# Performance work log

Measured on AMD Instinct MI355X. Metric: run time of the kernel, lower is better.

The kernel has to match this reference:

```python
import jax, jax.numpy as jnp
import numpy as np

BETA = 0.25
GAMMA = 0.9
EPS = 1e-05
B, H, W, D, K = 64, 32, 32, 256, 1024


def setup_inputs() -> dict:
    key = jax.random.key(0)
    k1, k2 = jax.random.split(key)
    return {
        "inputs": jax.random.normal(k1, (B, H, W, D), dtype=jnp.float32),
        "codebook": jax.random.normal(k2, (D, K), dtype=jnp.float32),
        "ema_hidden_cluster": jnp.zeros((K,), dtype=jnp.float32),
        "ema_hidden_dw": jnp.zeros((D, K), dtype=jnp.float32),
        "counter": 1,  # counter after increment (fresh state: 0 + 1)
    }


def reference(inputs, codebook, ema_hidden_cluster, ema_hidden_dw, counter):
    d, k = codebook.shape
    flat = inputs.reshape(-1, d)  # [N, D]
    distances = (
        jnp.sum(jnp.square(flat), 1, keepdims=True)
        - 2.0 * jnp.matmul(flat, codebook)
        + jnp.sum(jnp.square(codebook), 0, keepdims=True)
    )
    encoding_indices = jnp.argmin(distances, axis=1)  # [N]
    encodings = jax.nn.one_hot(encoding_indices, k, dtype=distances.dtype)  # [N, K]
    flat_quantized = jnp.take(codebook, encoding_indices, axis=1).swapaxes(1, 0)  # [N, D]
    quantized = flat_quantized.reshape(inputs.shape)
    loss = BETA * jnp.mean(jnp.square(jax.lax.stop_gradient(quantized) - inputs))

    # --- EMA codebook update (training=True path) ---
    decay = jnp.float32(GAMMA)
    one = jnp.float32(1.0)
    bias = one - jnp.power(decay, counter)
    cluster_size = jnp.sum(encodings, axis=0)  # [K]
    hid_cs = ema_hidden_cluster * decay + cluster_size * (one - decay)
    avg_cs = hid_cs / bias
    dw = jnp.matmul(flat.T, encodings)  # [D, K]
    hid_dw = ema_hidden_dw * decay + dw * (one - decay)
    avg_dw = hid_dw / bias
    n = jnp.sum(avg_cs)
    smoothed_cs = (avg_cs + EPS) / (n + k * EPS) * n
    new_codebook = avg_dw / smoothed_cs[None, :]

    ste = inputs + jax.lax.stop_gradient(quantized - inputs)
    avg_probs = jnp.mean(encodings, 0)
    perplexity = jnp.exp(-jnp.sum(avg_probs * jnp.log(avg_probs + 1e-10)))
    return (ste, perplexity, loss, new_codebook)
```

## Files before the change

### kernel.cpp

```cpp
#include <hip/hip_runtime.h>

#define N 65536
#define D 256
#define K 1024
#define BETA 0.25f
#define GAMMA 0.9f
#define EPS 1e-5f

#define DWROWS 64

#define OFF_INDICES 0
#define OFF_PERM    262144
#define OFF_COUNTS  524288
#define OFF_CNORM   528384
#define OFF_OFFSETS 532480
#define OFF_CURSOR  536576
#define OFF_SMOOTH  540672
#define OFF_LOSSP   544768
#define OFF_CBT     546816
#define OFF_CBE     1595392

typedef __bf16 bf16x8 __attribute__((ext_vector_type(8)));
typedef short  s16x8  __attribute__((ext_vector_type(8)));
typedef float  f32x4  __attribute__((ext_vector_type(4)));

__device__ inline unsigned short f32_to_bf16_rn(float f) {
    unsigned int u = __float_as_uint(f);
    unsigned int r = u + 0x7fffu + ((u >> 16) & 1u);
    return (unsigned short)(r >> 16);
}

__device__ inline f32x4 mfma16(s16x8 a, s16x8 b, f32x4 c) {
    return __builtin_amdgcn_mfma_f32_16x16x32_bf16(
        __builtin_bit_cast(bf16x8, a), __builtin_bit_cast(bf16x8, b), c, 0, 0, 0);
}

__device__ __forceinline__ void stage16(const s16x8* __restrict__ g, s16x8* l) {
    __builtin_amdgcn_global_load_lds(
        (const __attribute__((address_space(1))) void*)g,
        (__attribute__((address_space(3))) void*)l, 16, 0, 0);
}

__global__ __launch_bounds__(256) void pack_cb(const float* __restrict__ cb,
                                               float* __restrict__ cbT,
                                               s16x8* __restrict__ cbEp,
                                               float* __restrict__ cnorm) {
    const int ct = blockIdx.x >> 2;
    const int c2 = blockIdx.x & 3;
#pragma unroll
    for (int it = 0; it < 2; ++it) {
        int u = it * 256 + threadIdx.x;
        int frgc = u >> 7;
        int ks = (u >> 6) & 1;
        int L = u & 63;
        int c = ct * 64 + frgc * 16 + (L & 15);
        int d0 = c2 * 64 + (ks * 4 + (L >> 4)) * 8;
        float v[8];
        s16x8 hv, lv;
        float ss = 0.f;
#pragma unroll
        for (int j = 0; j < 8; ++j) {
            float f = cb[(size_t)(d0 + j) * K + c];
            v[j] = f;
            unsigned short h = f32_to_bf16_rn(f);
            hv[j] = (short)h;
            lv[j] = (short)f32_to_bf16_rn(f - __uint_as_float((unsigned)h << 16));
            ss = fmaf(f, f, ss);
        }
        *(float4*)&cbT[(size_t)c * D + d0]     = make_float4(v[0], v[1], v[2], v[3]);
        *(float4*)&cbT[(size_t)c * D + d0 + 4] = make_float4(v[4], v[5], v[6], v[7]);
        cbEp[(size_t)(ct * 8 + c2) * 512 + u]     = hv;
        cbEp[(size_t)(ct * 8 + 4 + c2) * 512 + u] = lv;
        atomicAdd(&cnorm[c], ss);
    }
}

__global__ __launch_bounds__(256, 2) void argmin_mfma_kernel(
        const float* __restrict__ x,
        const s16x8* __restrict__ cbEp,
        const float* __restrict__ cnorm,
        int* __restrict__ indices,
        int* __restrict__ counts) {
    __shared__ s16x8 Bs[2][1024];

    const int tid = threadIdx.x;
    const int lane = tid & 63;
    const int w = tid >> 6;
    const int r0 = blockIdx.x * 128;
    const int row16 = lane & 15;
    const int quad = lane >> 4;

#pragma unroll
    for (int i = 0; i < 4; ++i)
        stage16(cbEp + i * 256 + tid, &Bs[0][i * 256 + w * 64]);

    s16x8 Ah[2][8], Al[2][8];
#pragma unroll
    for (int frg = 0; frg < 2; ++frg) {
#pragma unroll
        for (int kb8 = 0; kb8 < 8; ++kb8) {
            const float* src = &x[(size_t)(r0 + w * 32 + frg * 16 + row16) * D
                                  + kb8 * 32 + quad * 8];
            float4 v0 = *(const float4*)src;
            float4 v1 = *(const float4*)(src + 4);
            float f[8] = {v0.x, v0.y, v0.z, v0.w, v1.x, v1.y, v1.z, v1.w};
            s16x8 hv, lv;
#pragma unroll
            for (int j = 0; j < 8; ++j) {
                unsigned short h = f32_to_bf16_rn(f[j]);
                hv[j] = (short)h;
                lv[j] = (short)f32_to_bf16_rn(f[j] - __uint_as_float((unsigned)h << 16));
            }
            Ah[frg][kb8] = hv;
            Al[frg][kb8] = lv;
        }
    }

    float minv[2][4];
    int   mini[2][4];
#pragma unroll
    for (int frg = 0; frg < 2; ++frg)
#pragma unroll
        for (int reg = 0; reg < 4; ++reg) { minv[frg][reg] = 3.4e38f; mini[frg][reg] = 0; }

    for (int ct = 0; ct < 16; ++ct) {
        f32x4 acc[2][4];
#pragma unroll
        for (int frg = 0; frg < 2; ++frg)
#pragma unroll
            for (int fc = 0; fc < 4; ++fc) acc[frg][fc] = (f32x4){0.f, 0.f, 0.f, 0.f};

#pragma unroll
        for (int ph = 0; ph < 4; ++ph) {
            __syncthreads();
            const bool has_next = !(ct == 15 && ph == 3);
            if (has_next) {
                const int nct = (ph == 3) ? ct + 1 : ct;
                const int nph = (ph == 3) ? 0 : ph + 1;
                const size_t gb = (size_t)(nct * 8 + nph * 2) * 512;
#pragma unroll
                for (int i = 0; i < 4; ++i)
                    stage16(cbEp + gb + i * 256 + tid, &Bs[(ph + 1) & 1][i * 256 + w * 64]);
            }
#pragma unroll
            for (int half = 0; half < 2; ++half) {
                const int cchunk = ph * 2 + half;
                const int c2 = cchunk & 3;
#pragma unroll
                for (int ks = 0; ks < 2; ++ks) {
                    const int ksb = c2 * 2 + ks;
#pragma unroll
                    for (int fc = 0; fc < 4; ++fc) {
                        s16x8 b = Bs[ph & 1][half * 512 + (fc * 2 + ks) * 64 + lane];
#pragma unroll
                        for (int frg = 0; frg < 2; ++frg) {
                            acc[frg][fc] = mfma16(Ah[frg][ksb], b, acc[frg][fc]);
                            if (cchunk < 4)
                                acc[frg][fc] = mfma16(Al[frg][ksb], b, acc[frg][fc]);
                        }
                    }
                }
            }
        }
#pragma unroll
        for (int fc = 0; fc < 4; ++fc) {
            int col = ct * 64 + fc * 16 + row16;
            float cn = cnorm[col];
#pragma unroll
            for (int frg = 0; frg < 2; ++frg)
#pragma unroll
                for (int reg = 0; reg < 4; ++reg) {
                    float val = fmaf(-2.f, acc[frg][fc][reg], cn);
                    if (val < minv[frg][reg]) { minv[frg][reg] = val; mini[frg][reg] = col; }
                }
        }
    }

#pragma unroll
    for (int mask = 1; mask <= 8; mask <<= 1) {
#pragma unroll
        for (int frg = 0; frg < 2; ++frg)
#pragma unroll
            for (int reg = 0; reg < 4; ++reg) {
                float ov = __shfl_xor(minv[frg][reg], mask, 64);
                int   oi = __shfl_xor(mini[frg][reg], mask, 64);
                if (ov < minv[frg][reg] ||
                    (ov == minv[frg][reg] && oi < mini[frg][reg])) {
                    minv[frg][reg] = ov; mini[frg][reg] = oi;
                }
            }
    }
    if (row16 == 0) {
#pragma unroll
        for (int frg = 0; frg < 2; ++frg)
#pragma unroll
            for (int reg = 0; reg < 4; ++reg) {
                const int idx = mini[frg][reg];
                indices[r0 + w * 32 + frg * 16 + quad * 4 + reg] = idx;
                atomicAdd(&counts[idx], 1);
            }
    }
}

__global__ __launch_bounds__(1024) void finalize_kernel(const int* __restrict__ counts,
                                                        const float* __restrict__ ema_c,
                                                        const int* __restrict__ counter,
                                                        float* __restrict__ out_perp,
                                                        int* __restrict__ cursor,
                                                        float* __restrict__ smoothed) {
    const int k = threadIdx.x;
    __shared__ float fred[1024];
    __shared__ int scan[1024];
    __shared__ float nsum_s;

    const int c = counts[k];
    const float bias = 1.0f - powf(GAMMA, (float)counter[0]);
    const float hid = fmaf(ema_c[k], GAMMA, (float)c * (1.0f - GAMMA));
    const float avg = hid / bias;

    fred[k] = avg;
    __syncthreads();
    for (int s = 512; s >= 1; s >>= 1) {
        if (k < s) fred[k] += fred[k + s];
        __syncthreads();
    }
    if (k == 0) nsum_s = fred[0];
    __syncthreads();
    const float nsum = nsum_s;

    float p = (float)c * (1.0f / (float)N);
    fred[k] = p * logf(p + 1e-10f);
    __syncthreads();
    for (int s = 512; s >= 1; s >>= 1) {
        if (k < s) fred[k] += fred[k + s];
        __syncthreads();
    }
    if (k == 0) out_perp[0] = expf(-fred[0]);

    scan[k] = c;
    __syncthreads();
    for (int s = 1; s < 1024; s <<= 1) {
        int v = (k >= s) ? scan[k - s] : 0;
        __syncthreads();
        scan[k] += v;
        __syncthreads();
    }
    cursor[k] = scan[k] - c;

    smoothed[k] = (avg + EPS) / (nsum + (float)K * EPS) * nsum;
}

__global__ __launch_bounds__(256) void scatter_kernel(const int* __restrict__ indices,
                                                      int* __restrict__ cursor,
                                                      int* __restrict__ permk,
                                                      float* __restrict__ dwT) {
    const int n = blockIdx.x * 256 + threadIdx.x;
    *(float4*)&dwT[(size_t)n * 4] = make_float4(0.f, 0.f, 0.f, 0.f);
    const int k = indices[n];
    const int pos = atomicAdd(&cursor[k], 1);
    permk[pos] = n | (k << 16);
}

__global__ __launch_bounds__(256) void dw_fused_kernel(const float* __restrict__ x,
                                                       const float* __restrict__ cbT,
                                                       const int* __restrict__ permk,
                                                       float* __restrict__ ste,
                                                       float* __restrict__ dwT,
                                                       float* __restrict__ lossp) {
    __shared__ int s_rows[DWROWS];
    __shared__ int s_keys[DWROWS + 1];
    const int d = threadIdx.x;
    const int base = blockIdx.x * DWROWS;
    if (threadIdx.x < DWROWS) {
        const int pk = permk[base + threadIdx.x];
        s_rows[threadIdx.x] = pk & 0xffff;
        s_keys[threadIdx.x] = pk >> 16;
    }
    if (threadIdx.x == 0) s_keys[DWROWS] = -1;
    __syncthreads();
    float acc = 0.f;
    float ls = 0.f;
#pragma unroll 4
    for (int i = 0; i < DWROWS; ++i) {
        const int n = s_rows[i];
        const int k = s_keys[i];
        const float xv = x[(size_t)n * D + d];
        const float q  = cbT[(size_t)k * D + d];
        ste[(size_t)n * D + d] = q;
        acc += xv;
        const float df = q - xv;
        ls = fmaf(df, df, ls);
        if (s_keys[i + 1] != k) {
            atomicAdd(&dwT[(size_t)k * D + d], acc);
            acc = 0.f;
        }
    }
#pragma unroll
    for (int off = 32; off >= 1; off >>= 1) ls += __shfl_down(ls, off, 64);
    __shared__ float red[4];
    if ((d & 63) == 0) red[d >> 6] = ls;
    __syncthreads();
    if (d == 0) lossp[blockIdx.x] = red[0] + red[1] + red[2] + red[3];
}

__global__ __launch_bounds__(256) void codebook_final_kernel(const float* __restrict__ dwT,
                                                             const float* __restrict__ ema_dw,
                                                             const float* __restrict__ smoothed,
                                                             const int* __restrict__ counter,
                                                             const float* __restrict__ lossp,
                                                             float* __restrict__ out_cb,
                                                             float* __restrict__ out_loss) {
    __shared__ float tile[64][65];
    __shared__ float lred[4];
    const int tid = threadIdx.x;

    if (blockIdx.x == 0) {
        float s = lossp[tid] + lossp[tid + 256] + lossp[tid + 512] + lossp[tid + 768];
#pragma unroll
        for (int off = 32; off >= 1; off >>= 1) s += __shfl_down(s, off, 64);
        if ((tid & 63) == 0) lred[tid >> 6] = s;
        __syncthreads();
        if (tid == 0)
            out_loss[0] = BETA * (lred[0] + lred[1] + lred[2] + lred[3])
                          * (1.0f / ((float)N * (float)D));
        __syncthreads();
    }

    const int d0 = (blockIdx.x & 3) * 64;
    const int k0 = (blockIdx.x >> 2) * 64;
#pragma unroll
    for (int it = 0; it < 16; ++it) {
        int idx = it * 256 + tid;
        int kk = idx >> 6, dd = idx & 63;
        tile[kk][dd] = dwT[(size_t)(k0 + kk) * D + d0 + dd];
    }
    __syncthreads();
    const float bias = 1.0f - powf(GAMMA, (float)counter[0]);
#pragma unroll
    for (int it = 0; it < 16; ++it) {
        int idx = it * 256 + tid;
        int dd = idx >> 6, kk = idx & 63;
        float dwv = tile[kk][dd];
        float hid = fmaf(ema_dw[(size_t)(d0 + dd) * K + k0 + kk], GAMMA,
                         dwv * (1.0f - GAMMA));
        out_cb[(size_t)(d0 + dd) * K + k0 + kk] = (hid / bias) / smoothed[k0 + kk];
    }
}

extern "C" void kernel_launch(void* const* d_in, const int* in_sizes, int n_in,
                              void* d_out, int out_size, void* d_ws, size_t ws_size,
                              hipStream_t stream) {
    const float* x       = (const float*)d_in[0];
    const float* cb      = (const float*)d_in[1];
    const float* ema_c   = (const float*)d_in[2];
    const float* ema_dw  = (const float*)d_in[3];
    const int*   counter = (const int*)d_in[4];

    float* out = (float*)d_out;
    float* ste = out;
    float* out_perp = out + (size_t)N * D;
    float* out_loss = out_perp + 1;
    float* out_cb = out_perp + 2;

    char* ws = (char*)d_ws;
    int* indices  = (int*)(ws + OFF_INDICES);
    int* permk    = (int*)(ws + OFF_PERM);
    int* counts   = (int*)(ws + OFF_COUNTS);
    float* cnorm  = (float*)(ws + OFF_CNORM);
    int* cursor   = (int*)(ws + OFF_CURSOR);
    float* smooth = (float*)(ws + OFF_SMOOTH);
    float* cbT    = (float*)(ws + OFF_CBT);
    s16x8* cbEp   = (s16x8*)(ws + OFF_CBE);
    float* dwT    = (float*)(ws + OFF_CBE);
    float* lossp  = (float*)(ws + OFF_CNORM);

    hipMemsetAsync(counts, 0, 2 * K * sizeof(int), stream);

    pack_cb<<<64, 256, 0, stream>>>(cb, cbT, cbEp, cnorm);
    argmin_mfma_kernel<<<N / 128, 256, 0, stream>>>(x, cbEp, cnorm, indices, counts);
    finalize_kernel<<<1, 1024, 0, stream>>>(counts, ema_c, counter,
                                            out_perp, cursor, smooth);
    scatter_kernel<<<N / 256, 256, 0, stream>>>(indices, cursor, permk, dwT);
    dw_fused_kernel<<<N / DWROWS, 256, 0, stream>>>(x, cbT, permk, ste, dwT, lossp);
    codebook_final_kernel<<<64, 256, 0, stream>>>(dwT, ema_dw, smooth, counter,
                                                  lossp, out_cb, out_loss);
}
```

Before: 311.2 us.

## Replace sort-based dw accumulation with direct atomic scatter and fuse finalize

Removes the counting-sort pipeline (finalize scan, scatter, permuted dw kernel) and replaces it with one grid-stride kernel where each wavefront handles one row: it gathers the codeword into ste, atomically adds x into dwT per element, and counts cluster hits. The smoothing and perplexity reductions move into every codebook_final block, and the dwT zeroing becomes a memset. This cuts two kernel launches and the permutation traffic, but turns segment-reduced atomics into one float atomic per element (N*D atomics), which can contend heavily on popular codewords.

```diff
diff --git a/kernel.cpp b/kernel.cpp
--- a/kernel.cpp
+++ b/kernel.cpp
@@ -7,7 +7,7 @@
 #define GAMMA 0.9f
 #define EPS 1e-5f
 
-#define DWROWS 64
+#define TBLOCKS 512
 
 #define OFF_INDICES 0
 #define OFF_PERM    262144
@@ -79,8 +79,7 @@
         const float* __restrict__ x,
         const s16x8* __restrict__ cbEp,
         const float* __restrict__ cnorm,
-        int* __restrict__ indices,
-        int* __restrict__ counts) {
+        int* __restrict__ indices) {
     __shared__ s16x8 Bs[2][1024];
 
     const int tid = threadIdx.x;
@@ -194,136 +193,98 @@
 #pragma unroll
         for (int frg = 0; frg < 2; ++frg)
 #pragma unroll
-            for (int reg = 0; reg < 4; ++reg) {
-                const int idx = mini[frg][reg];
-                indices[r0 + w * 32 + frg * 16 + quad * 4 + reg] = idx;
-                atomicAdd(&counts[idx], 1);
-            }
-    }
-}
-
-__global__ __launch_bounds__(1024) void finalize_kernel(const int* __restrict__ counts,
-                                                        const float* __restrict__ ema_c,
-                                                        const int* __restrict__ counter,
-                                                        float* __restrict__ out_perp,
-                                                        int* __restrict__ cursor,
-                                                        float* __restrict__ smoothed) {
-    const int k = threadIdx.x;
-    __shared__ float fred[1024];
-    __shared__ int scan[1024];
-    __shared__ float nsum_s;
-
-    const int c = counts[k];
-    const float bias = 1.0f - powf(GAMMA, (float)counter[0]);
-    const float hid = fmaf(ema_c[k], GAMMA, (float)c * (1.0f - GAMMA));
-    const float avg = hid / bias;
-
-    fred[k] = avg;
-    __syncthreads();
-    for (int s = 512; s >= 1; s >>= 1) {
-        if (k < s) fred[k] += fred[k + s];
-        __syncthreads();
-    }
-    if (k == 0) nsum_s = fred[0];
-    __syncthreads();
-    const float nsum = nsum_s;
-
-    float p = (float)c * (1.0f / (float)N);
-    fred[k] = p * logf(p + 1e-10f);
-    __syncthreads();
-    for (int s = 512; s >= 1; s >>= 1) {
-        if (k < s) fred[k] += fred[k + s];
-        __syncthreads();
-    }
-    if (k == 0) out_perp[0] = expf(-fred[0]);
-
-    scan[k] = c;
-    __syncthreads();
-    for (int s = 1; s < 1024; s <<= 1) {
-        int v = (k >= s) ? scan[k - s] : 0;
-        __syncthreads();
-        scan[k] += v;
-        __syncthreads();
-    }
-    cursor[k] = scan[k] - c;
-
-    smoothed[k] = (avg + EPS) / (nsum + (float)K * EPS) * nsum;
-}
-
-__global__ __launch_bounds__(256) void scatter_kernel(const int* __restrict__ indices,
-                                                      int* __restrict__ cursor,
-                                                      int* __restrict__ permk,
-                                                      float* __restrict__ dwT) {
-    const int n = blockIdx.x * 256 + threadIdx.x;
-    *(float4*)&dwT[(size_t)n * 4] = make_float4(0.f, 0.f, 0.f, 0.f);
-    const int k = indices[n];
-    const int pos = atomicAdd(&cursor[k], 1);
-    permk[pos] = n | (k << 16);
-}
-
-__global__ __launch_bounds__(256) void dw_fused_kernel(const float* __restrict__ x,
-                                                       const float* __restrict__ cbT,
-                                                       const int* __restrict__ permk,
-                                                       float* __restrict__ ste,
-                                                       float* __restrict__ dwT,
-                                                       float* __restrict__ lossp) {
-    __shared__ int s_rows[DWROWS];
-    __shared__ int s_keys[DWROWS + 1];
-    const int d = threadIdx.x;
-    const int base = blockIdx.x * DWROWS;
-    if (threadIdx.x < DWROWS) {
-        const int pk = permk[base + threadIdx.x];
-        s_rows[threadIdx.x] = pk & 0xffff;
-        s_keys[threadIdx.x] = pk >> 16;
-    }
-    if (threadIdx.x == 0) s_keys[DWROWS] = -1;
-    __syncthreads();
-    float acc = 0.f;
+            for (int reg = 0; reg < 4; ++reg)
+                indices[r0 + w * 32 + frg * 16 + quad * 4 + reg] = mini[frg][reg];
+    }
+}
+
+__global__ __launch_bounds__(256) void tail_fused_kernel(const float* __restrict__ x,
+                                                         const float* __restrict__ cbT,
+                                                         const int* __restrict__ indices,
+                                                         float* __restrict__ ste,
+                                                         float* __restrict__ dwT,
+                                                         int* __restrict__ counts,
+                                                         float* __restrict__ lossp) {
+    const int lane = threadIdx.x & 63;
+    const int wid = (blockIdx.x * 256 + threadIdx.x) >> 6;
+    const int nwaves = TBLOCKS * 4;
+
     float ls = 0.f;
-#pragma unroll 4
-    for (int i = 0; i < DWROWS; ++i) {
-        const int n = s_rows[i];
-        const int k = s_keys[i];
-        const float xv = x[(size_t)n * D + d];
-        const float q  = cbT[(size_t)k * D + d];
-        ste[(size_t)n * D + d] = q;
-        acc += xv;
-        const float df = q - xv;
-        ls = fmaf(df, df, ls);
-        if (s_keys[i + 1] != k) {
-            atomicAdd(&dwT[(size_t)k * D + d], acc);
-            acc = 0.f;
-        }
+    for (int row = wid; row < N; row += nwaves) {
+        const int k = indices[row];
+        float4 q  = *(const float4*)&cbT[(size_t)k * D + lane * 4];
+        float4 xi = *(const float4*)&x[(size_t)row * D + lane * 4];
+        *(float4*)&ste[(size_t)row * D + lane * 4] = q;
+        float* dst = &dwT[(size_t)k * D + lane * 4];
+        atomicAdd(dst + 0, xi.x);
+        atomicAdd(dst + 1, xi.y);
+        atomicAdd(dst + 2, xi.z);
+        atomicAdd(dst + 3, xi.w);
+        float dx = q.x - xi.x, dy = q.y - xi.y, dz = q.z - xi.z, dw = q.w - xi.w;
+        ls = fmaf(dx, dx, ls); ls = fmaf(dy, dy, ls);
+        ls = fmaf(dz, dz, ls); ls = fmaf(dw, dw, ls);
+        if (lane == 0) atomicAdd(&counts[k], 1);
     }
 #pragma unroll
     for (int off = 32; off >= 1; off >>= 1) ls += __shfl_down(ls, off, 64);
     __shared__ float red[4];
-    if ((d & 63) == 0) red[d >> 6] = ls;
+    if ((threadIdx.x & 63) == 0) red[threadIdx.x >> 6] = ls;
     __syncthreads();
-    if (d == 0) lossp[blockIdx.x] = red[0] + red[1] + red[2] + red[3];
+    if (threadIdx.x == 0)
+        lossp[blockIdx.x] = red[0] + red[1] + red[2] + red[3];
 }
 
 __global__ __launch_bounds__(256) void codebook_final_kernel(const float* __restrict__ dwT,
                                                              const float* __restrict__ ema_dw,
-                                                             const float* __restrict__ smoothed,
+                                                             const int* __restrict__ counts,
+                                                             const float* __restrict__ ema_c,
                                                              const int* __restrict__ counter,
                                                              const float* __restrict__ lossp,
                                                              float* __restrict__ out_cb,
-                                                             float* __restrict__ out_loss) {
+                                                             float* __restrict__ out_loss,
+                                                             float* __restrict__ out_perp) {
     __shared__ float tile[64][65];
+    __shared__ float sm[1024];
+    __shared__ float wred[4][2];
     __shared__ float lred[4];
     const int tid = threadIdx.x;
+    const float bias = 1.0f - powf(GAMMA, (float)counter[0]);
+
+    float avg4[4];
+    float a = 0.f, e = 0.f;
+#pragma unroll
+    for (int i = 0; i < 4; ++i) {
+        const int k = i * 256 + tid;
+        const int c = counts[k];
+        const float avg = fmaf(ema_c[k], GAMMA, (float)c * (1.0f - GAMMA)) / bias;
+        avg4[i] = avg;
+        a += avg;
+        const float p = (float)c * (1.0f / (float)N);
+        e += p * logf(p + 1e-10f);
+    }
+#pragma unroll
+    for (int off = 32; off >= 1; off >>= 1) {
+        a += __shfl_down(a, off, 64);
+        e += __shfl_down(e, off, 64);
+    }
+    if ((tid & 63) == 0) { wred[tid >> 6][0] = a; wred[tid >> 6][1] = e; }
+    __syncthreads();
+    const float nsum = wred[0][0] + wred[1][0] + wred[2][0] + wred[3][0];
+#pragma unroll
+    for (int i = 0; i < 4; ++i)
+        sm[i * 256 + tid] = (avg4[i] + EPS) / (nsum + (float)K * EPS) * nsum;
 
     if (blockIdx.x == 0) {
-        float s = lossp[tid] + lossp[tid + 256] + lossp[tid + 512] + lossp[tid + 768];
+        float s = lossp[tid] + lossp[tid + 256];
 #pragma unroll
         for (int off = 32; off >= 1; off >>= 1) s += __shfl_down(s, off, 64);
         if ((tid & 63) == 0) lred[tid >> 6] = s;
         __syncthreads();
-        if (tid == 0)
+        if (tid == 0) {
             out_loss[0] = BETA * (lred[0] + lred[1] + lred[2] + lred[3])
                           * (1.0f / ((float)N * (float)D));
-        __syncthreads();
+            out_perp[0] = expf(-(wred[0][1] + wred[1][1] + wred[2][1] + wred[3][1]));
+        }
     }
 
     const int d0 = (blockIdx.x & 3) * 64;
@@ -335,7 +296,6 @@
         tile[kk][dd] = dwT[(size_t)(k0 + kk) * D + d0 + dd];
     }
     __syncthreads();
-    const float bias = 1.0f - powf(GAMMA, (float)counter[0]);
 #pragma unroll
     for (int it = 0; it < 16; ++it) {
         int idx = it * 256 + tid;
@@ -343,7 +303,7 @@
         float dwv = tile[kk][dd];
         float hid = fmaf(ema_dw[(size_t)(d0 + dd) * K + k0 + kk], GAMMA,
                          dwv * (1.0f - GAMMA));
-        out_cb[(size_t)(d0 + dd) * K + k0 + kk] = (hid / bias) / smoothed[k0 + kk];
+        out_cb[(size_t)(d0 + dd) * K + k0 + kk] = (hid / bias) / sm[k0 + kk];
     }
 }
 
@@ -364,11 +324,8 @@
 
     char* ws = (char*)d_ws;
     int* indices  = (int*)(ws + OFF_INDICES);
-    int* permk    = (int*)(ws + OFF_PERM);
     int* counts   = (int*)(ws + OFF_COUNTS);
     float* cnorm  = (float*)(ws + OFF_CNORM);
-    int* cursor   = (int*)(ws + OFF_CURSOR);
-    float* smooth = (float*)(ws + OFF_SMOOTH);
     float* cbT    = (float*)(ws + OFF_CBT);
     s16x8* cbEp   = (s16x8*)(ws + OFF_CBE);
     float* dwT    = (float*)(ws + OFF_CBE);
@@ -377,11 +334,11 @@
     hipMemsetAsync(counts, 0, 2 * K * sizeof(int), stream);
 
     pack_cb<<<64, 256, 0, stream>>>(cb, cbT, cbEp, cnorm);
-    argmin_mfma_kernel<<<N / 128, 256, 0, stream>>>(x, cbEp, cnorm, indices, counts);
-    finalize_kernel<<<1, 1024, 0, stream>>>(counts, ema_c, counter,
-                                            out_perp, cursor, smooth);
-    scatter_kernel<<<N / 256, 256, 0, stream>>>(indices, cursor, permk, dwT);
-    dw_fused_kernel<<<N / DWROWS, 256, 0, stream>>>(x, cbT, permk, ste, dwT, lossp);
-    codebook_final_kernel<<<64, 256, 0, stream>>>(dwT, ema_dw, smooth, counter,
-                                                  lossp, out_cb, out_loss);
-}
+    argmin_mfma_kernel<<<N / 128, 256, 0, stream>>>(x, cbEp, cnorm, indices);
+    hipMemsetAsync(dwT, 0, (size_t)K * D * sizeof(float), stream);
+    tail_fused_kernel<<<TBLOCKS, 256, 0, stream>>>(x, cbT, indices, ste, dwT,
+                                                   counts, lossp);
+    codebook_final_kernel<<<64, 256, 0, stream>>>(dwT, ema_dw, counts, ema_c,
+                                                  counter, lossp, out_cb,
+                                                  out_loss, out_perp);
+}
```

After: 706.8 us. 2.27x slower.
